# Kernel optimization log

Measured on AMD Instinct MI355X. Metric: run time of the kernel, lower is better.

Reference implementation:

```python
import jax, jax.numpy as jnp
import numpy as np
from jax import lax

LEADS = 61
BETA = 2.0
DN = ('NCHW', 'OIHW', 'NCHW')


def setup_inputs() -> dict:
    key = jax.random.key(0)
    ks = jax.random.split(key, 11)
    B, L = 128, LEADS
    w = lambda k, shape: jax.random.normal(k, shape, jnp.float32) * 0.1
    return {
        "x": jax.random.normal(ks[0], (B, L, 32, 250), jnp.float32),
        "w1": w(ks[1], (L, 8, 1, 3, 4)),   "b1": w(ks[2], (L, 8)),
        "w2": w(ks[3], (L, 16, 8, 4, 3)),  "b2": w(ks[4], (L, 16)),
        "w3": w(ks[5], (L, 32, 16, 3, 4)), "b3": w(ks[6], (L, 32)),
        "w4": w(ks[7], (L, 64, 32, 2, 4)), "b4": w(ks[8], (L, 64)),
        "fcw": w(ks[9], (L, 3, 64)),       "fcb": w(ks[10], (L, 3)),
    }


def _maxpool2(h):
    return lax.reduce_window(h, -jnp.inf, lax.max, (1, 1, 2, 2), (1, 1, 2, 2), 'VALID')


def _lead(x, w1, b1, w2, b2, w3, b3, w4, b4, fcw, fcb):
    # x: (B,1,32,250) for a single lead; weights for that lead only
    h = lax.conv_general_dilated(x, w1, (1, 2), [(1, 1), (2, 2)], dimension_numbers=DN) + b1[None, :, None, None]
    h = jax.nn.relu(_maxpool2(h))                                  # (B,8,16,63)
    h = lax.conv_general_dilated(h, w2, (2, 2), [(1, 1), (1, 1)], dimension_numbers=DN) + b2[None, :, None, None]
    h = jax.nn.relu(_maxpool2(h))                                  # (B,16,4,16)
    h = lax.conv_general_dilated(h, w3, (1, 2), [(1, 1), (1, 1)], dimension_numbers=DN) + b3[None, :, None, None]
    h = jax.nn.relu(_maxpool2(h))                                  # (B,32,2,4)
    h = lax.conv_general_dilated(h, w4, (1, 1), 'VALID', dimension_numbers=DN) + b4[None, :, None, None]  # (B,64,1,1)
    h = h.reshape(h.shape[0], 64)
    logits = h @ fcw.T + fcb                                       # (B,3)
    return jax.nn.softmax(logits, axis=-1)


def reference(x, w1, b1, w2, b2, w3, b3, w4, b4, fcw, fcb):
    # batch all 61 per-lead pipelines via vmap over the lead axis
    xl = jnp.transpose(x, (1, 0, 2, 3))[:, :, None]                # (L,B,1,32,250)
    preds = jax.vmap(_lead)(xl, w1, b1, w2, b2, w3, b3, w4, b4, fcw, fcb)  # (L,B,3)
    preds = jnp.transpose(preds, (1, 0, 2))                        # (B,L,3)
    # eval-mode multiplicative fusion loss (Liu et al.)
    one_m = 1.0 - preds
    prod_all = jnp.prod(one_m, axis=1, keepdims=True)              # prod over all leads
    coeff = lax.stop_gradient(prod_all / one_m)                    # prod over k != j (detached)
    beta_exp = BETA / (LEADS - 1)
    loss = -jnp.sum(coeff ** beta_exp * jnp.log(preds), axis=1)    # (B,3)
    return loss
```

## Files before the change

### kernel.cpp

```cpp
#include <hip/hip_runtime.h>
#include <math.h>
#include <utility>

#define NLEADS 61
#define AIL __attribute__((always_inline))

template <int... Is, typename F>
__device__ __forceinline__ void sf_(std::integer_sequence<int, Is...>, F&& f) {
    (f(std::integral_constant<int, Is>{}), ...);
}
template <int N, typename F>
__device__ __forceinline__ void static_for(F&& f) {
    sf_(std::make_integer_sequence<int, N>{}, (F&&)f);
}

__device__ __forceinline__ float4 ld4(const float* p) { return *(const float4*)p; }
__device__ __forceinline__ float2 ld2(const float* p) { return *(const float2*)p; }

template <int C> __device__ __forceinline__ float f4c(float4 v) {
    if constexpr (C == 0) return v.x;
    else if constexpr (C == 1) return v.y;
    else if constexpr (C == 2) return v.z;
    else return v.w;
}
template <int C> __device__ __forceinline__ float f6(float4 a, float2 b) {
    if constexpr (C < 4) return f4c<C>(a);
    else if constexpr (C == 4) return b.x;
    else return b.y;
}
template <int K> __device__ __forceinline__ float w12(float4 w0, float4 w1, float4 w2) {
    if constexpr (K < 4) return f4c<K>(w0);
    else if constexpr (K < 8) return f4c<K - 4>(w1);
    else return f4c<K - 8>(w2);
}

__global__ __launch_bounds__(256, 4)
void lead_cnn_kernel(const float* __restrict__ x,
                     const float* __restrict__ w1g, const float* __restrict__ b1g,
                     const float* __restrict__ w2g, const float* __restrict__ b2g,
                     const float* __restrict__ w3g, const float* __restrict__ b3g,
                     const float* __restrict__ w4g, const float* __restrict__ b4g,
                     const float* __restrict__ fcwg, const float* __restrict__ fcbg,
                     float* __restrict__ preds)
{
    __shared__ __align__(16) float smem[10060];
    float* const A  = smem;
    float* const H2 = smem + 8704;
    float* const ZR = smem + 9992;

    const int t = threadIdx.x;
    const int b = blockIdx.x;
    const int l = blockIdx.y;

    const float* xg  = x + ((size_t)b * NLEADS + l) * 8000;
    const float* w1l = w1g + l * 96;
    const float* b1l = b1g + l * 8;

    if (t < 68) ZR[t] = 0.f;
    for (int i = t; i < 640; i += 256) {
        const int ch = i / 80, j = i - ch * 80;
        const int r = j / 5, k = j - r * 5;
        A[ch * 1088 + r * 68 + ((k == 0) ? 0 : (63 + k))] = 0.f;
    }
    for (int i = t; i < 128; i += 256) {
        const int ch = i >> 3, r = (i >> 1) & 3;
        H2[ch * 80 + r * 20 + ((i & 1) ? 17 : 0)] = 0.f;
    }

    static_for<4>([&](auto IT) AIL {
        constexpr int it = IT.value;
        const int item = t + it * 256;
        int ph = item / 63;
        const int pw = item - ph * 63;
        const bool valid = (ph < 16);
        ph = valid ? ph : 15;
        const int c1 = (pw == 0) ? 0 : (4 * pw - 2);
        const int c3 = (pw >= 62) ? 248 : (4 * pw + 2);
        const bool lok = (pw > 0), rok = (pw < 62);
        float xw[24];
        {
            const bool ok = (ph > 0);
            const float* xr = xg + (ok ? (2 * ph - 1) : 0) * 250;
            const float2 e0 = ld2(xr + c1);
            const float2 e1 = ld2(xr + 4 * pw);
            const float2 e2 = ld2(xr + c3);
            const bool okl = ok & lok, okr = ok & rok;
            xw[0] = okl ? e0.x : 0.f;  xw[1] = okl ? e0.y : 0.f;
            xw[2] = ok  ? e1.x : 0.f;  xw[3] = ok  ? e1.y : 0.f;
            xw[4] = okr ? e2.x : 0.f;  xw[5] = okr ? e2.y : 0.f;
        }
        static_for<2>([&](auto RR) AIL {
            constexpr int r = RR.value + 1;
            const float* xr = xg + (2 * ph - 1 + r) * 250;
            const float2 e0 = ld2(xr + c1);
            const float2 e1 = ld2(xr + 4 * pw);
            const float2 e2 = ld2(xr + c3);
            xw[r*6+0] = lok ? e0.x : 0.f;  xw[r*6+1] = lok ? e0.y : 0.f;
            xw[r*6+2] = e1.x;              xw[r*6+3] = e1.y;
            xw[r*6+4] = rok ? e2.x : 0.f;  xw[r*6+5] = rok ? e2.y : 0.f;
        });
        {
            const bool ok = (ph < 15);
            const float* xr = xg + (ok ? (2 * ph + 2) : 31) * 250;
            const float2 e0 = ld2(xr + c1);
            const float2 e1 = ld2(xr + 4 * pw);
            const float2 e2 = ld2(xr + c3);
            const bool okl = ok & lok, okr = ok & rok;
            xw[18] = okl ? e0.x : 0.f;  xw[19] = okl ? e0.y : 0.f;
            xw[20] = ok  ? e1.x : 0.f;  xw[21] = ok  ? e1.y : 0.f;
            xw[22] = okr ? e2.x : 0.f;  xw[23] = okr ? e2.y : 0.f;
        }
        const int sbase = ph * 68 + pw + 1;
        static_for<8>([&](auto OC) AIL {
            constexpr int oc = OC.value;
            const float4 q0 = ld4(w1l + oc * 12);
            const float4 q1 = ld4(w1l + oc * 12 + 4);
            const float4 q2 = ld4(w1l + oc * 12 + 8);
            float p00 = 0.f, p01 = 0.f, p10 = 0.f, p11 = 0.f;
            static_for<3>([&](auto KH) AIL {
                constexpr int kh = KH.value;
                static_for<4>([&](auto KW) AIL {
                    constexpr int kw = KW.value;
                    const float wv = w12<kh * 4 + kw>(q0, q1, q2);
                    p00 = fmaf(wv, xw[kh * 6 + kw], p00);
                    p01 = fmaf(wv, xw[kh * 6 + kw + 2], p01);
                    p10 = fmaf(wv, xw[(kh + 1) * 6 + kw], p10);
                    p11 = fmaf(wv, xw[(kh + 1) * 6 + kw + 2], p11);
                });
            });
            const float m = fmaxf(fmaxf(p00, p01), fmaxf(p10, p11));
            if (valid) A[oc * 1088 + sbase] = fmaxf(m + b1l[oc], 0.f);
        });
    });
    __syncthreads();

    {
        const int s2 = t & 63;
        const int ogu = __builtin_amdgcn_readfirstlane(t >> 6);
        const int ph2 = s2 >> 4, pw2 = s2 & 15;
        float a2[16];
        static_for<16>([&](auto I) AIL { a2[I.value] = 0.f; });
        static_for<8>([&](auto IC) AIL {
            constexpr int ic = IC.value;
            float4 ya[6]; float2 yb[6];
            static_for<6>([&](auto R) AIL {
                constexpr int r = R.value;
                const int Rr = 4 * ph2 - 1 + r;
                const float* hp;
                if constexpr (r == 0) {
                    hp = (ph2 > 0) ? (A + ic * 1088 + Rr * 68 + 4 * pw2) : (ZR + 4 * pw2);
                } else if constexpr (r == 5) {
                    hp = (ph2 < 3) ? (A + ic * 1088 + Rr * 68 + 4 * pw2) : (ZR + 4 * pw2);
                } else {
                    hp = A + ic * 1088 + Rr * 68 + 4 * pw2;
                }
                ya[r] = ld4(hp); yb[r] = ld2(hp + 4);
            });
            static_for<4>([&](auto OL) AIL {
                constexpr int ol = OL.value;
                const float* wp = w2g + ((size_t)((l * 16 + ogu * 4 + ol) * 8 + ic)) * 12;
                const float4 q0 = ld4(wp), q1 = ld4(wp + 4), q2 = ld4(wp + 8);
                static_for<4>([&](auto KH) AIL {
                    constexpr int kh = KH.value;
                    static_for<3>([&](auto KW) AIL {
                        constexpr int kw = KW.value;
                        const float wv = w12<kh * 3 + kw>(q0, q1, q2);
                        a2[ol*4+0] = fmaf(wv, f6<kw>(ya[kh], yb[kh]), a2[ol*4+0]);
                        a2[ol*4+1] = fmaf(wv, f6<kw + 2>(ya[kh], yb[kh]), a2[ol*4+1]);
                        a2[ol*4+2] = fmaf(wv, f6<kw>(ya[kh + 2], yb[kh + 2]), a2[ol*4+2]);
                        a2[ol*4+3] = fmaf(wv, f6<kw + 2>(ya[kh + 2], yb[kh + 2]), a2[ol*4+3]);
                    });
                });
            });
        });
        static_for<4>([&](auto OL) AIL {
            constexpr int ol = OL.value;
            const int oc = ogu * 4 + ol;
            const float m = fmaxf(fmaxf(a2[ol*4+0], a2[ol*4+1]),
                                  fmaxf(a2[ol*4+2], a2[ol*4+3]));
            H2[oc * 80 + ph2 * 20 + pw2 + 1] = fmaxf(m + b2g[l * 16 + oc], 0.f);
        });
    }
    __syncthreads();

    {
        const int oc3 = t >> 3, s3 = t & 7;
        const int ph3 = s3 >> 2, pw3 = s3 & 3;
        const float* w3l = w3g + (size_t)l * 6144 + oc3 * 192;
        const float b3v = b3g[l * 32 + oc3];
        float a30 = 0.f, a31 = 0.f, a32 = 0.f, a33 = 0.f;
        static_for<16>([&](auto IC) AIL {
            constexpr int ic = IC.value;
            float4 za[4]; float2 zb[4];
            static_for<4>([&](auto R) AIL {
                constexpr int r = R.value;
                const int Rr = 2 * ph3 - 1 + r;
                const float* zp;
                if constexpr (r == 0) {
                    zp = (ph3 > 0) ? (H2 + ic * 80 + Rr * 20 + 4 * pw3) : (ZR + 4 * pw3);
                } else if constexpr (r == 3) {
                    zp = (ph3 < 1) ? (H2 + ic * 80 + Rr * 20 + 4 * pw3) : (ZR + 4 * pw3);
                } else {
                    zp = H2 + ic * 80 + Rr * 20 + 4 * pw3;
                }
                za[r] = ld4(zp); zb[r] = ld2(zp + 4);
            });
            const float4 q0 = ld4(w3l + ic * 12);
            const float4 q1 = ld4(w3l + ic * 12 + 4);
            const float4 q2 = ld4(w3l + ic * 12 + 8);
            static_for<3>([&](auto KH) AIL {
                constexpr int kh = KH.value;
                static_for<4>([&](auto KW) AIL {
                    constexpr int kw = KW.value;
                    const float wv = w12<kh * 4 + kw>(q0, q1, q2);
                    a30 = fmaf(wv, f6<kw>(za[kh], zb[kh]), a30);
                    a31 = fmaf(wv, f6<kw + 2>(za[kh], zb[kh]), a31);
                    a32 = fmaf(wv, f6<kw>(za[kh + 1], zb[kh + 1]), a32);
                    a33 = fmaf(wv, f6<kw + 2>(za[kh + 1], zb[kh + 1]), a33);
                });
            });
        });
        const float m = fmaxf(fmaxf(a30, a31), fmaxf(a32, a33));
        A[oc3 * 8 + s3] = fmaxf(m + b3v, 0.f);
    }
    __syncthreads();

    {
        if (t < 192) A[600 + t] = fcwg[l * 192 + t];
        else if (t < 195) A[600 + t] = fcbg[l * 3 + (t - 192)];

        const int oc4 = t >> 2, part = t & 3;
        const float* w4p = w4g + (size_t)l * 16384 + oc4 * 256 + part * 64;
        float s4 = 0.f;
        static_for<8>([&](auto J) AIL {
            constexpr int j = J.value;
            const float4 wa = ld4(w4p + j * 8);
            const float4 wb = ld4(w4p + j * 8 + 4);
            const float* xx = A + (part * 8 + j) * 8;
            const float4 xA = ld4(xx), xB = ld4(xx + 4);
            s4 = fmaf(wa.x, xA.x, s4); s4 = fmaf(wa.y, xA.y, s4);
            s4 = fmaf(wa.z, xA.z, s4); s4 = fmaf(wa.w, xA.w, s4);
            s4 = fmaf(wb.x, xB.x, s4); s4 = fmaf(wb.y, xB.y, s4);
            s4 = fmaf(wb.z, xB.z, s4); s4 = fmaf(wb.w, xB.w, s4);
        });
        A[256 + part * 64 + oc4] = s4;
    }
    __syncthreads();
    if (t < 64)
        A[512 + t] = A[256 + t] + A[320 + t] + A[384 + t] + A[448 + t]
                   + b4g[l * 64 + t];
    __syncthreads();

    if (t < 3) {
        float s = A[792 + t];
        static_for<64>([&](auto I) AIL {
            s = fmaf(A[600 + t * 64 + I.value], A[512 + I.value], s);
        });
        A[580 + t] = s;
    }
    __syncthreads();
    if (t == 0) {
        const float a0 = A[580], a1 = A[581], a2 = A[582];
        const float m = fmaxf(a0, fmaxf(a1, a2));
        const float e0 = expf(a0 - m), e1 = expf(a1 - m), e2 = expf(a2 - m);
        const float inv = 1.f / (e0 + e1 + e2);
        float* pr = preds + ((size_t)b * NLEADS + l) * 3;
        pr[0] = e0 * inv; pr[1] = e1 * inv; pr[2] = e2 * inv;
    }
}

__global__ void fusion_loss_kernel(const float* __restrict__ preds,
                                   float* __restrict__ out, int B)
{
    const int idx = blockIdx.x * blockDim.x + threadIdx.x;
    if (idx >= B * 3) return;
    const int b = idx / 3;
    const int c = idx - 3 * b;
    const float* p = preds + (size_t)b * (NLEADS * 3) + c;
    float S = 0.f;
    for (int j = 0; j < NLEADS; ++j) S += logf(1.f - p[j * 3]);
    const float be = 2.0f / 60.0f;
    float loss = 0.f;
    for (int j = 0; j < NLEADS; ++j) {
        const float pj = p[j * 3];
        loss += expf(be * (S - logf(1.f - pj))) * logf(pj);
    }
    out[idx] = -loss;
}

extern "C" void kernel_launch(void* const* d_in, const int* in_sizes, int n_in,
                              void* d_out, int out_size, void* d_ws, size_t ws_size,
                              hipStream_t stream)
{
    const float* x   = (const float*)d_in[0];
    const float* w1  = (const float*)d_in[1];
    const float* b1  = (const float*)d_in[2];
    const float* w2  = (const float*)d_in[3];
    const float* b2  = (const float*)d_in[4];
    const float* w3  = (const float*)d_in[5];
    const float* b3  = (const float*)d_in[6];
    const float* w4  = (const float*)d_in[7];
    const float* b4  = (const float*)d_in[8];
    const float* fcw = (const float*)d_in[9];
    const float* fcb = (const float*)d_in[10];

    const int B = in_sizes[0] / (NLEADS * 32 * 250);
    float* preds = (float*)d_ws;

    dim3 grid(B, NLEADS);
    hipLaunchKernelGGL(lead_cnn_kernel, grid, dim3(256), 0, stream,
                       x, w1, b1, w2, b2, w3, b3, w4, b4, fcw, fcb, preds);

    const int total = B * 3;
    hipLaunchKernelGGL(fusion_loss_kernel, dim3((total + 255) / 256), dim3(256),
                       0, stream, preds, (float*)d_out, B);
}
```

Baseline: 529.5 us.

## Compute two pooled rows per thread in conv1 and double-buffer conv2/conv3 loads

Conv1 now has each thread handle two vertically adjacent pooled outputs, using a 6-row input window instead of two 4-row windows. This cuts redundant global loads of overlapping input rows and reduces the work items from four iterations to two per thread. Conv2 and conv3 load the next input channel's LDS data, and for conv3 also its weights, into a second register buffer while computing the current channel, so LDS latency overlaps with FMAs. In exchange, register pressure rises (two 36-float windows and duplicated buffers), which may lower occupancy.

```diff
diff --git a/kernel.cpp b/kernel.cpp
--- a/kernel.cpp
+++ b/kernel.cpp
@@ -67,20 +67,23 @@
         H2[ch * 80 + r * 20 + ((i & 1) ? 17 : 0)] = 0.f;
     }
 
-    static_for<4>([&](auto IT) AIL {
-        constexpr int it = IT.value;
-        const int item = t + it * 256;
-        int ph = item / 63;
-        const int pw = item - ph * 63;
-        const bool valid = (ph < 16);
-        ph = valid ? ph : 15;
+    const int item0 = t;
+    const int item1 = t + 256;
+    const int php0 = item0 / 63, pw0 = item0 - php0 * 63;
+    int       php1 = item1 / 63;
+    const int pw1  = item1 - php1 * 63;
+    const bool valid1 = (item1 < 504);
+    php1 = valid1 ? php1 : 7;
+
+    float xwA[36], xwB[36];
+
+    auto ldx = [&](float (&xw)[36], const int php, const int pw) AIL {
         const int c1 = (pw == 0) ? 0 : (4 * pw - 2);
         const int c3 = (pw >= 62) ? 248 : (4 * pw + 2);
         const bool lok = (pw > 0), rok = (pw < 62);
-        float xw[24];
         {
-            const bool ok = (ph > 0);
-            const float* xr = xg + (ok ? (2 * ph - 1) : 0) * 250;
+            const bool ok = (php > 0);
+            const float* xr = xg + (ok ? (4 * php - 1) : 0) * 250;
             const float2 e0 = ld2(xr + c1);
             const float2 e1 = ld2(xr + 4 * pw);
             const float2 e2 = ld2(xr + c3);
@@ -89,73 +92,99 @@
             xw[2] = ok  ? e1.x : 0.f;  xw[3] = ok  ? e1.y : 0.f;
             xw[4] = okr ? e2.x : 0.f;  xw[5] = okr ? e2.y : 0.f;
         }
-        static_for<2>([&](auto RR) AIL {
-            constexpr int r = RR.value + 1;
-            const float* xr = xg + (2 * ph - 1 + r) * 250;
+        static_for<4>([&](auto RR) AIL {
+            constexpr int lr = RR.value + 1;
+            const float* xr = xg + (4 * php - 1 + lr) * 250;
             const float2 e0 = ld2(xr + c1);
             const float2 e1 = ld2(xr + 4 * pw);
             const float2 e2 = ld2(xr + c3);
-            xw[r*6+0] = lok ? e0.x : 0.f;  xw[r*6+1] = lok ? e0.y : 0.f;
-            xw[r*6+2] = e1.x;              xw[r*6+3] = e1.y;
-            xw[r*6+4] = rok ? e2.x : 0.f;  xw[r*6+5] = rok ? e2.y : 0.f;
+            xw[lr*6+0] = lok ? e0.x : 0.f;  xw[lr*6+1] = lok ? e0.y : 0.f;
+            xw[lr*6+2] = e1.x;              xw[lr*6+3] = e1.y;
+            xw[lr*6+4] = rok ? e2.x : 0.f;  xw[lr*6+5] = rok ? e2.y : 0.f;
         });
         {
-            const bool ok = (ph < 15);
-            const float* xr = xg + (ok ? (2 * ph + 2) : 31) * 250;
+            const bool ok = (php < 7);
+            const float* xr = xg + (ok ? (4 * php + 4) : 31) * 250;
             const float2 e0 = ld2(xr + c1);
             const float2 e1 = ld2(xr + 4 * pw);
             const float2 e2 = ld2(xr + c3);
             const bool okl = ok & lok, okr = ok & rok;
-            xw[18] = okl ? e0.x : 0.f;  xw[19] = okl ? e0.y : 0.f;
-            xw[20] = ok  ? e1.x : 0.f;  xw[21] = ok  ? e1.y : 0.f;
-            xw[22] = okr ? e2.x : 0.f;  xw[23] = okr ? e2.y : 0.f;
+            xw[30] = okl ? e0.x : 0.f;  xw[31] = okl ? e0.y : 0.f;
+            xw[32] = ok  ? e1.x : 0.f;  xw[33] = ok  ? e1.y : 0.f;
+            xw[34] = okr ? e2.x : 0.f;  xw[35] = okr ? e2.y : 0.f;
         }
-        const int sbase = ph * 68 + pw + 1;
+    };
+
+    ldx(xwA, php0, pw0);
+    ldx(xwB, php1, pw1);
+
+    auto cmp1 = [&](const float (&xw)[36], const int php, const int pw,
+                    const bool dostore) AIL {
+        const int sb = (2 * php) * 68 + pw + 1;
         static_for<8>([&](auto OC) AIL {
             constexpr int oc = OC.value;
             const float4 q0 = ld4(w1l + oc * 12);
             const float4 q1 = ld4(w1l + oc * 12 + 4);
             const float4 q2 = ld4(w1l + oc * 12 + 8);
-            float p00 = 0.f, p01 = 0.f, p10 = 0.f, p11 = 0.f;
+            float p[8];
+            static_for<8>([&](auto I) AIL { p[I.value] = 0.f; });
             static_for<3>([&](auto KH) AIL {
                 constexpr int kh = KH.value;
                 static_for<4>([&](auto KW) AIL {
                     constexpr int kw = KW.value;
                     const float wv = w12<kh * 4 + kw>(q0, q1, q2);
-                    p00 = fmaf(wv, xw[kh * 6 + kw], p00);
-                    p01 = fmaf(wv, xw[kh * 6 + kw + 2], p01);
-                    p10 = fmaf(wv, xw[(kh + 1) * 6 + kw], p10);
-                    p11 = fmaf(wv, xw[(kh + 1) * 6 + kw + 2], p11);
+                    static_for<4>([&](auto J) AIL {
+                        constexpr int j = J.value;
+                        p[j*2+0] = fmaf(wv, xw[(j + kh) * 6 + kw],     p[j*2+0]);
+                        p[j*2+1] = fmaf(wv, xw[(j + kh) * 6 + kw + 2], p[j*2+1]);
+                    });
                 });
             });
-            const float m = fmaxf(fmaxf(p00, p01), fmaxf(p10, p11));
-            if (valid) A[oc * 1088 + sbase] = fmaxf(m + b1l[oc], 0.f);
-        });
-    });
+            const float m0 = fmaxf(fmaxf(p[0], p[1]), fmaxf(p[2], p[3]));
+            const float m1 = fmaxf(fmaxf(p[4], p[5]), fmaxf(p[6], p[7]));
+            const float v0 = fmaxf(m0 + b1l[oc], 0.f);
+            const float v1 = fmaxf(m1 + b1l[oc], 0.f);
+            if (dostore) {
+                A[oc * 1088 + sb]      = v0;
+                A[oc * 1088 + sb + 68] = v1;
+            }
+        });
+    };
+    cmp1(xwA, php0, pw0, true);
+    cmp1(xwB, php1, pw1, valid1);
     __syncthreads();
 
     {
         const int s2 = t & 63;
         const int ogu = __builtin_amdgcn_readfirstlane(t >> 6);
         const int ph2 = s2 >> 4, pw2 = s2 & 15;
+        struct Buf2 { float4 ya[6]; float2 yb[6]; };
+        Buf2 bA, bB;
+        const float* const Pz = ZR + 4 * pw2;
+        const float* const Pm = A + (4 * ph2 - 1) * 68 + 4 * pw2;
+
+        auto ldic = [&](auto ICC, Buf2& bb) AIL {
+            constexpr int ic = ICC.value;
+            {
+                const float* hp = (ph2 > 0) ? (Pm + ic * 1088) : Pz;
+                bb.ya[0] = ld4(hp); bb.yb[0] = ld2(hp + 4);
+            }
+            static_for<4>([&](auto RR) AIL {
+                constexpr int r = RR.value + 1;
+                const float* hp = Pm + ic * 1088 + r * 68;
+                bb.ya[r] = ld4(hp); bb.yb[r] = ld2(hp + 4);
+            });
+            {
+                const float* hp = (ph2 < 3) ? (Pm + ic * 1088 + 5 * 68) : Pz;
+                bb.ya[5] = ld4(hp); bb.yb[5] = ld2(hp + 4);
+            }
+        };
+
         float a2[16];
         static_for<16>([&](auto I) AIL { a2[I.value] = 0.f; });
-        static_for<8>([&](auto IC) AIL {
-            constexpr int ic = IC.value;
-            float4 ya[6]; float2 yb[6];
-            static_for<6>([&](auto R) AIL {
-                constexpr int r = R.value;
-                const int Rr = 4 * ph2 - 1 + r;
-                const float* hp;
-                if constexpr (r == 0) {
-                    hp = (ph2 > 0) ? (A + ic * 1088 + Rr * 68 + 4 * pw2) : (ZR + 4 * pw2);
-                } else if constexpr (r == 5) {
-                    hp = (ph2 < 3) ? (A + ic * 1088 + Rr * 68 + 4 * pw2) : (ZR + 4 * pw2);
-                } else {
-                    hp = A + ic * 1088 + Rr * 68 + 4 * pw2;
-                }
-                ya[r] = ld4(hp); yb[r] = ld2(hp + 4);
-            });
+
+        auto cmpic = [&](auto ICC, const Buf2& bb) AIL {
+            constexpr int ic = ICC.value;
             static_for<4>([&](auto OL) AIL {
                 constexpr int ol = OL.value;
                 const float* wp = w2g + ((size_t)((l * 16 + ogu * 4 + ol) * 8 + ic)) * 12;
@@ -165,14 +194,26 @@
                     static_for<3>([&](auto KW) AIL {
                         constexpr int kw = KW.value;
                         const float wv = w12<kh * 3 + kw>(q0, q1, q2);
-                        a2[ol*4+0] = fmaf(wv, f6<kw>(ya[kh], yb[kh]), a2[ol*4+0]);
-                        a2[ol*4+1] = fmaf(wv, f6<kw + 2>(ya[kh], yb[kh]), a2[ol*4+1]);
-                        a2[ol*4+2] = fmaf(wv, f6<kw>(ya[kh + 2], yb[kh + 2]), a2[ol*4+2]);
-                        a2[ol*4+3] = fmaf(wv, f6<kw + 2>(ya[kh + 2], yb[kh + 2]), a2[ol*4+3]);
+                        a2[ol*4+0] = fmaf(wv, f6<kw>(bb.ya[kh], bb.yb[kh]), a2[ol*4+0]);
+                        a2[ol*4+1] = fmaf(wv, f6<kw + 2>(bb.ya[kh], bb.yb[kh]), a2[ol*4+1]);
+                        a2[ol*4+2] = fmaf(wv, f6<kw>(bb.ya[kh + 2], bb.yb[kh + 2]), a2[ol*4+2]);
+                        a2[ol*4+3] = fmaf(wv, f6<kw + 2>(bb.ya[kh + 2], bb.yb[kh + 2]), a2[ol*4+3]);
                     });
                 });
             });
-        });
+        };
+
+        ldic(std::integral_constant<int, 0>{}, bA);
+        static_for<8>([&](auto IC) AIL {
+            constexpr int ic = IC.value;
+            if constexpr (ic < 7) {
+                if constexpr ((ic + 1) & 1) ldic(std::integral_constant<int, ic + 1>{}, bB);
+                else                        ldic(std::integral_constant<int, ic + 1>{}, bA);
+            }
+            if constexpr (ic & 1) cmpic(IC, bB);
+            else                  cmpic(IC, bA);
+        });
+
         static_for<4>([&](auto OL) AIL {
             constexpr int ol = OL.value;
             const int oc = ogu * 4 + ol;
@@ -188,38 +229,57 @@
         const int ph3 = s3 >> 2, pw3 = s3 & 3;
         const float* w3l = w3g + (size_t)l * 6144 + oc3 * 192;
         const float b3v = b3g[l * 32 + oc3];
+        struct Buf3 { float4 za[4]; float2 zb[4]; float4 q0, q1, q2; };
+        Buf3 cA, cB;
+        const float* const Pz = ZR + 4 * pw3;
+        const float* const Pm = H2 + (2 * ph3 - 1) * 20 + 4 * pw3;
+
+        auto ldic3 = [&](auto ICC, Buf3& bb) AIL {
+            constexpr int ic = ICC.value;
+            {
+                const float* zp = (ph3 > 0) ? (Pm + ic * 80) : Pz;
+                bb.za[0] = ld4(zp); bb.zb[0] = ld2(zp + 4);
+            }
+            static_for<2>([&](auto RR) AIL {
+                constexpr int r = RR.value + 1;
+                const float* zp = Pm + ic * 80 + r * 20;
+                bb.za[r] = ld4(zp); bb.zb[r] = ld2(zp + 4);
+            });
+            {
+                const float* zp = (ph3 < 1) ? (Pm + ic * 80 + 3 * 20) : Pz;
+                bb.za[3] = ld4(zp); bb.zb[3] = ld2(zp + 4);
+            }
+            bb.q0 = ld4(w3l + ic * 12);
+            bb.q1 = ld4(w3l + ic * 12 + 4);
+            bb.q2 = ld4(w3l + ic * 12 + 8);
+        };
+
         float a30 = 0.f, a31 = 0.f, a32 = 0.f, a33 = 0.f;
-        static_for<16>([&](auto IC) AIL {
-            constexpr int ic = IC.value;
-            float4 za[4]; float2 zb[4];
-            static_for<4>([&](auto R) AIL {
-                constexpr int r = R.value;
-                const int Rr = 2 * ph3 - 1 + r;
-                const float* zp;
-                if constexpr (r == 0) {
-                    zp = (ph3 > 0) ? (H2 + ic * 80 + Rr * 20 + 4 * pw3) : (ZR + 4 * pw3);
-                } else if constexpr (r == 3) {
-                    zp = (ph3 < 1) ? (H2 + ic * 80 + Rr * 20 + 4 * pw3) : (ZR + 4 * pw3);
-                } else {
-                    zp = H2 + ic * 80 + Rr * 20 + 4 * pw3;
-                }
-                za[r] = ld4(zp); zb[r] = ld2(zp + 4);
-            });
-            const float4 q0 = ld4(w3l + ic * 12);
-            const float4 q1 = ld4(w3l + ic * 12 + 4);
-            const float4 q2 = ld4(w3l + ic * 12 + 8);
+        auto cmpic3 = [&](const Buf3& bb) AIL {
             static_for<3>([&](auto KH) AIL {
                 constexpr int kh = KH.value;
                 static_for<4>([&](auto KW) AIL {
                     constexpr int kw = KW.value;
-                    const float wv = w12<kh * 4 + kw>(q0, q1, q2);
-                    a30 = fmaf(wv, f6<kw>(za[kh], zb[kh]), a30);
-                    a31 = fmaf(wv, f6<kw + 2>(za[kh], zb[kh]), a31);
-                    a32 = fmaf(wv, f6<kw>(za[kh + 1], zb[kh + 1]), a32);
-                    a33 = fmaf(wv, f6<kw + 2>(za[kh + 1], zb[kh + 1]), a33);
+                    const float wv = w12<kh * 4 + kw>(bb.q0, bb.q1, bb.q2);
+                    a30 = fmaf(wv, f6<kw>(bb.za[kh], bb.zb[kh]), a30);
+                    a31 = fmaf(wv, f6<kw + 2>(bb.za[kh], bb.zb[kh]), a31);
+                    a32 = fmaf(wv, f6<kw>(bb.za[kh + 1], bb.zb[kh + 1]), a32);
+                    a33 = fmaf(wv, f6<kw + 2>(bb.za[kh + 1], bb.zb[kh + 1]), a33);
                 });
             });
-        });
+        };
+
+        ldic3(std::integral_constant<int, 0>{}, cA);
+        static_for<16>([&](auto IC) AIL {
+            constexpr int ic = IC.value;
+            if constexpr (ic < 15) {
+                if constexpr ((ic + 1) & 1) ldic3(std::integral_constant<int, ic + 1>{}, cB);
+                else                        ldic3(std::integral_constant<int, ic + 1>{}, cA);
+            }
+            if constexpr (ic & 1) cmpic3(cB);
+            else                  cmpic3(cA);
+        });
+
         const float m = fmaxf(fmaxf(a30, a31), fmaxf(a32, a33));
         A[oc3 * 8 + s3] = fmaxf(m + b3v, 0.f);
     }
```

Result: no change. 525.3 us (-0.8%).
